# Optimization experiments

Measured on AMD Instinct MI355X. Metric: run time of the kernel, lower is better.

## Reference

```python
import jax, jax.numpy as jnp
import numpy as np

B, T, C = 4, 2048, 768   # batch, seq, n_embd
E, K = 8, 2              # n_routed_experts, moe_top_k (expert hidden dim == C per source)


def setup_inputs() -> dict:
    key = jax.random.key(0)
    ks = jax.random.split(key, 6)
    s = 0.02  # init scale to keep relu(x)^2 well-behaved
    return {
        "x": jax.random.normal(ks[0], (B, T, C), jnp.float32),
        "w_fc_sh": jax.random.normal(ks[1], (C, C), jnp.float32) * s,    # shared expert c_fc (stored [in,out])
        "w_proj_sh": jax.random.normal(ks[2], (C, C), jnp.float32) * s,  # shared expert c_proj
        "w1": jax.random.normal(ks[3], (E, C, C), jnp.float32) * s,      # routed experts c_fc, [E,in,out]
        "w2": jax.random.normal(ks[4], (E, C, C), jnp.float32) * s,      # routed experts c_proj
        "router_w": jax.random.normal(ks[5], (E, C), jnp.float32) * s,   # router weight [E, C]
        "balance_bias": jnp.zeros((E,), jnp.float32),                    # router balance_bias buffer
    }


def _mlp(x, wfc, wproj):
    # MLP: c_proj(relu(c_fc(x))**2)
    h = jnp.square(jax.nn.relu(x @ wfc))
    return h @ wproj


def reference(x, w_fc_sh, w_proj_sh, w1, w2, router_w, balance_bias):
    Bx, Tx, Cx = x.shape
    shared = _mlp(x, w_fc_sh, w_proj_sh)                    # [B,T,C]

    xf = x.reshape(-1, Cx)                                  # [N,C]
    # --- router ---
    logits = xf.astype(jnp.float32) @ router_w.T            # [N,E]
    scores = jax.nn.sigmoid(logits)
    _, idx = jax.lax.top_k(scores + balance_bias, K)        # selection uses biased scores
    tw = jnp.take_along_axis(scores, idx, axis=-1)          # gate weights from unbiased scores
    tw = tw / (tw.sum(-1, keepdims=True) + 1e-20)           # [N,K]

    # per-token per-expert combine weights (equivalent to gather/MLP/index_add loop)
    combine = (jax.nn.one_hot(idx, E, dtype=tw.dtype) * tw[..., None]).sum(1)  # [N,E]

    # dense all-expert compute, masked combine (same math as sparse dispatch)
    h = jnp.square(jax.nn.relu(jnp.einsum('nc,ech->neh', xf, w1)))  # [N,E,H]
    y = jnp.einsum('neh,ehc->nec', h, w2)                            # [N,E,C]
    routed = jnp.einsum('nec,ne->nc', y, combine)                    # [N,C]

    return shared + routed.reshape(Bx, Tx, Cx)
```

## Files before the change

kernel.cpp:

```cpp
#include <hip/hip_runtime.h>
#include <stdint.h>

#define N_TOK 8192
#define C_DIM 768
#define E_NUM 8
#define NT32 24
#define TOTX3 104
#define GRID3 312
#define XXP3 13

typedef short short8 __attribute__((ext_vector_type(8)));
typedef __bf16 bf16x8 __attribute__((ext_vector_type(8)));
typedef float f32x4 __attribute__((ext_vector_type(4)));

static __device__ __forceinline__ unsigned short f2bf(float f) {
    unsigned u = __float_as_uint(f);
    unsigned r = u + 0x7FFFu + ((u >> 16) & 1u);
    return (unsigned short)(r >> 16);
}
static __device__ __forceinline__ float bf2f(unsigned short h) {
    return __uint_as_float(((unsigned)h) << 16);
}

__global__ void wtrans_kernel(const float* __restrict__ wfc, const float* __restrict__ wpj,
                              const float* __restrict__ w1, const float* __restrict__ w2,
                              unsigned short* __restrict__ Wt) {
    __shared__ float tile[32][33];
    const int m = blockIdx.z;
    const float* src = (m == 0) ? wfc : (m == 1) ? wpj
                     : (m < 10) ? (w1 + (size_t)(m - 2) * C_DIM * C_DIM)
                                : (w2 + (size_t)(m - 10) * C_DIM * C_DIM);
    const int i0 = blockIdx.y * 32;
    const int o0 = blockIdx.x * 32;
    #pragma unroll
    for (int rr = 0; rr < 32; rr += 8)
        tile[threadIdx.y + rr][threadIdx.x] = src[(size_t)(i0 + threadIdx.y + rr) * C_DIM + o0 + threadIdx.x];
    __syncthreads();
    unsigned short* dst = Wt + (size_t)m * C_DIM * C_DIM;
    #pragma unroll
    for (int rr = 0; rr < 32; rr += 8) {
        int o = o0 + threadIdx.y + rr;
        dst[(size_t)o * C_DIM + i0 + threadIdx.x] = f2bf(tile[threadIdx.x][threadIdx.y + rr]);
    }
}

__global__ void router_kernel(const float* __restrict__ x, const float* __restrict__ rw,
                              const float* __restrict__ bias,
                              float* __restrict__ topk_w, int* __restrict__ eids,
                              unsigned short* __restrict__ xb) {
    const int wave = threadIdx.x >> 6;
    const int lane = threadIdx.x & 63;
    const int n = blockIdx.x * 4 + wave;
    const float* xp = x + (size_t)n * C_DIM + lane * 12;
    float xv[12];
    #pragma unroll
    for (int j = 0; j < 12; j++) xv[j] = xp[j];
    unsigned short* xbp = xb + (size_t)n * C_DIM + lane * 12;
    #pragma unroll
    for (int j = 0; j < 12; j++) xbp[j] = f2bf(xv[j]);
    float acc[E_NUM];
    #pragma unroll
    for (int e = 0; e < E_NUM; e++) acc[e] = 0.f;
    #pragma unroll
    for (int e = 0; e < E_NUM; e++) {
        const float* wp = rw + (size_t)e * C_DIM + lane * 12;
        #pragma unroll
        for (int j = 0; j < 12; j++) acc[e] += xv[j] * wp[j];
    }
    #pragma unroll
    for (int e = 0; e < E_NUM; e++) {
        #pragma unroll
        for (int off = 32; off > 0; off >>= 1) acc[e] += __shfl_xor(acc[e], off, 64);
    }
    if (lane == 0) {
        float sc[E_NUM];
        #pragma unroll
        for (int e = 0; e < E_NUM; e++) sc[e] = 1.f / (1.f + expf(-acc[e]));
        int e0 = 0; float best = -1e30f;
        #pragma unroll
        for (int e = 0; e < E_NUM; e++) { float v = sc[e] + bias[e]; if (v > best) { best = v; e0 = e; } }
        int e1 = -1; float best1 = -1e30f;
        #pragma unroll
        for (int e = 0; e < E_NUM; e++) { if (e == e0) continue; float v = sc[e] + bias[e]; if (v > best1) { best1 = v; e1 = e; } }
        float w0 = sc[e0], w1 = sc[e1];
        float s = w0 + w1 + 1e-20f;
        w0 /= s; w1 /= s;
        topk_w[n * 2] = w0; topk_w[n * 2 + 1] = w1;
        eids[n * 2] = e0; eids[n * 2 + 1] = e1;
    }
}

__global__ __launch_bounds__(1024) void bucketize_kernel(const int* __restrict__ eids,
                                                         int* __restrict__ counts,
                                                         int* __restrict__ buckets) {
    const int e = blockIdx.x;
    const int t = threadIdx.x;
    const int wv = t >> 6, lane = t & 63;
    __shared__ int wave_tot[16];
    int running = 0;
    for (int start = 0; start < 2 * N_TOK; start += 1024) {
        const int i = start + t;
        const int f = (eids[i] == e) ? 1 : 0;
        unsigned long long mask = __ballot(f);
        int pre = __popcll(mask & ((1ull << lane) - 1ull));
        if (lane == 0) wave_tot[wv] = __popcll(mask);
        __syncthreads();
        int wbase = 0, tot = 0;
        #pragma unroll
        for (int j = 0; j < 16; j++) { int c = wave_tot[j]; tot += c; if (j < wv) wbase += c; }
        if (f) buckets[e * N_TOK + running + wbase + pre] = i;
        running += tot;
        __syncthreads();
    }
    if (t == 0) counts[e] = running;
}

__global__ void prefix_kernel(const int* __restrict__ counts, int* __restrict__ xoffs) {
    if (threadIdx.x == 0 && blockIdx.x == 0) {
        int a = 0;
        for (int z = 0; z < E_NUM; z++) { xoffs[z] = a; a += (counts[z] + 255) >> 8; }
        xoffs[E_NUM] = a;
        xoffs[E_NUM + 1] = a + 32;
    }
}

#define GLOAD_LDS(g, l) __builtin_amdgcn_global_load_lds((const __attribute__((address_space(1))) void*)(g), (__attribute__((address_space(3))) void*)(l), 16, 0, 0)
#define WAITVM(n) asm volatile("s_waitcnt vmcnt(" #n ")" ::: "memory")
#define SCHEDB() __builtin_amdgcn_sched_barrier(0)
#define BAR() __builtin_amdgcn_s_barrier()

template <int PHASE>
__global__ __launch_bounds__(512, 2) void gemm_all_kernel(const unsigned short* __restrict__ Adir,
                                                          const unsigned short* __restrict__ Agat,
                                                          const unsigned short* __restrict__ WtAll,
                                                          void* __restrict__ dstDir,
                                                          unsigned short* __restrict__ dstGat,
                                                          const int* __restrict__ counts,
                                                          const int* __restrict__ buckets,
                                                          const int* __restrict__ xoffs) {
    const int fid = blockIdx.x;
    const int xcd = fid & 7;
    const int i3 = fid >> 3;
    const int xx = xcd * XXP3 + i3 / 3;
    const int y = i3 % 3;
    int xo[10];
    #pragma unroll
    for (int i = 0; i < 10; i++) xo[i] = xoffs[i];
    if (xx >= xo[9]) return;
    int z = E_NUM, xl = xx - xo[8];
    #pragma unroll
    for (int zz = 0; zz < E_NUM; zz++)
        if (xx >= xo[zz] && xx < xo[zz + 1]) { z = zz; xl = xx - xo[zz]; }
    const bool sh = (z == E_NUM);
    const int rows = sh ? N_TOK : counts[z];
    const int r0 = xl * 256;
    const int c0 = y * 256;

    __shared__ __align__(16) unsigned short lds[4 * 16384];

    const int t = threadIdx.x;
    const int lane = t & 63;
    const int wv = t >> 6;
    const int wm = wv >> 2;
    const int wn = wv & 3;

    const int widx = sh ? (PHASE == 0 ? 0 : 1) : (PHASE == 0 ? 2 + z : 10 + z);
    const unsigned short* Bmat = WtAll + (size_t)widx * C_DIM * C_DIM;
    const int* bk = buckets + z * N_TOK;

    const int srow = t >> 2;
    const int scol = (((t & 3) ^ ((t >> 3) & 3)) * 8);
    int grow0, grow1;
    const unsigned short* Asrc;
    if (sh) {
        Asrc = Adir;
        grow0 = r0 + srow; grow1 = r0 + 128 + srow;
    } else {
        Asrc = Agat;
        int p0 = r0 + srow, p1 = r0 + 128 + srow;
        int e0v = bk[p0 < rows ? p0 : 0];
        int e1v = bk[p1 < rows ? p1 : 0];
        grow0 = (PHASE == 0) ? (e0v >> 1) : e0v;
        grow1 = (PHASE == 0) ? (e1v >> 1) : e1v;
    }
    const unsigned short* ap0 = Asrc + (size_t)grow0 * C_DIM + scol;
    const unsigned short* ap1 = Asrc + (size_t)grow1 * C_DIM + scol;
    const unsigned short* bp0 = Bmat + (size_t)(c0 + srow) * C_DIM + scol;
    const unsigned short* bp1 = Bmat + (size_t)(c0 + 128 + srow) * C_DIM + scol;

    f32x4 acc[8][4];
    #pragma unroll
    for (int i = 0; i < 8; i++)
        #pragma unroll
        for (int j = 0; j < 4; j++) acc[i][j] = (f32x4){0.f, 0.f, 0.f, 0.f};

    const int fr = lane & 15;
    const int fq = lane >> 4;
    const int ks = ((fq ^ ((fr >> 1) & 3)) * 8);

    #pragma unroll
    for (int p = 0; p < 3; ++p) {
        unsigned short* d = lds + p * 16384 + t * 8;
        const int ko = p * 32;
        GLOAD_LDS(ap0 + ko, d);
        GLOAD_LDS(ap1 + ko, d + 4096);
        GLOAD_LDS(bp0 + ko, d + 8192);
        GLOAD_LDS(bp1 + ko, d + 12288);
    }

    #pragma unroll
    for (int kt = 0; kt < NT32; ++kt) {
        if (kt + 2 < NT32)      { WAITVM(8); }
        else if (kt + 1 < NT32) { WAITVM(4); }
        else                    { WAITVM(0); }
        BAR();
        SCHEDB();
        if (kt + 3 < NT32) {
            unsigned short* d = lds + ((kt + 3) & 3) * 16384 + t * 8;
            const int ko = (kt + 3) * 32;
            GLOAD_LDS(ap0 + ko, d);
            GLOAD_LDS(ap1 + ko, d + 4096);
            GLOAD_LDS(bp0 + ko, d + 8192);
            GLOAD_LDS(bp1 + ko, d + 12288);
        }
        SCHEDB();
        const unsigned short* buf = lds + (kt & 3) * 16384;
        short8 bfr[4];
        #pragma unroll
        for (int j = 0; j < 4; j++)
            bfr[j] = *reinterpret_cast<const short8*>(buf + 8192 + (size_t)(wn * 64 + j * 16 + fr) * 32 + ks);
        __builtin_amdgcn_s_setprio(1);
        #pragma unroll
        for (int i = 0; i < 8; i++) {
            short8 a = *reinterpret_cast<const short8*>(buf + (size_t)(wm * 128 + i * 16 + fr) * 32 + ks);
            #pragma unroll
            for (int j = 0; j < 4; j++)
                acc[i][j] = __builtin_amdgcn_mfma_f32_16x16x32_bf16(
                    __builtin_bit_cast(bf16x8, a), __builtin_bit_cast(bf16x8, bfr[j]), acc[i][j], 0, 0, 0);
        }
        __builtin_amdgcn_s_setprio(0);
    }

    const int orow = r0 + wm * 128;
    const int ocol = c0 + wn * 64;
    if (sh) {
        if constexpr (PHASE == 0) {
            unsigned short* Hd = (unsigned short*)dstDir;
            #pragma unroll
            for (int i = 0; i < 8; i++)
                #pragma unroll
                for (int rr = 0; rr < 4; rr++) {
                    size_t base = (size_t)(orow + i * 16 + fq * 4 + rr) * C_DIM;
                    #pragma unroll
                    for (int j = 0; j < 4; j++) {
                        float v = acc[i][j][rr];
                        float rl = v > 0.f ? v : 0.f;
                        Hd[base + ocol + j * 16 + fr] = f2bf(rl * rl);
                    }
                }
        } else {
            float* od = (float*)dstDir;
            #pragma unroll
            for (int i = 0; i < 8; i++)
                #pragma unroll
                for (int rr = 0; rr < 4; rr++) {
                    size_t base = (size_t)(orow + i * 16 + fq * 4 + rr) * C_DIM;
                    #pragma unroll
                    for (int j = 0; j < 4; j++)
                        od[base + ocol + j * 16 + fr] = acc[i][j][rr];
                }
        }
    } else {
        #pragma unroll
        for (int i = 0; i < 8; i++)
            #pragma unroll
            for (int rr = 0; rr < 4; rr++) {
                int pos = orow + i * 16 + fq * 4 + rr;
                if (pos < rows) {
                    int ent = bk[pos];
                    size_t base = (size_t)ent * C_DIM;
                    #pragma unroll
                    for (int j = 0; j < 4; j++) {
                        float v = acc[i][j][rr];
                        if (PHASE == 0) {
                            float rl = v > 0.f ? v : 0.f;
                            dstGat[base + ocol + j * 16 + fr] = f2bf(rl * rl);
                        } else {
                            dstGat[base + ocol + j * 16 + fr] = f2bf(v);
                        }
                    }
                }
            }
    }
}

__global__ void combine_kernel(float* __restrict__ out, const unsigned short* __restrict__ Y,
                               const float* __restrict__ tw) {
    int idx = blockIdx.x * blockDim.x + threadIdx.x;
    const int per_row = C_DIM / 4;
    if (idx >= N_TOK * per_row) return;
    int n = idx / per_row;
    int c = (idx % per_row) * 4;
    float w0 = tw[n * 2], w1 = tw[n * 2 + 1];
    const ushort4 a = *reinterpret_cast<const ushort4*>(Y + (size_t)(n * 2) * C_DIM + c);
    const ushort4 b = *reinterpret_cast<const ushort4*>(Y + (size_t)(n * 2 + 1) * C_DIM + c);
    float4* op = reinterpret_cast<float4*>(out + (size_t)n * C_DIM + c);
    float4 o = *op;
    o.x += w0 * bf2f(a.x) + w1 * bf2f(b.x);
    o.y += w0 * bf2f(a.y) + w1 * bf2f(b.y);
    o.z += w0 * bf2f(a.z) + w1 * bf2f(b.z);
    o.w += w0 * bf2f(a.w) + w1 * bf2f(b.w);
    *op = o;
}

extern "C" void kernel_launch(void* const* d_in, const int* in_sizes, int n_in,
                              void* d_out, int out_size, void* d_ws, size_t ws_size,
                              hipStream_t stream) {
    const float* x   = (const float*)d_in[0];
    const float* wfc = (const float*)d_in[1];
    const float* wpj = (const float*)d_in[2];
    const float* w1  = (const float*)d_in[3];
    const float* w2  = (const float*)d_in[4];
    const float* rw  = (const float*)d_in[5];
    const float* bias= (const float*)d_in[6];
    float* out = (float*)d_out;

    char* ws = (char*)d_ws;
    size_t off = 0;
    auto alloc = [&](size_t bytes) { void* p = ws + off; off += (bytes + 255) & ~(size_t)255; return p; };
    unsigned short* xb   = (unsigned short*)alloc((size_t)N_TOK * C_DIM * 2);
    unsigned short* Wt   = (unsigned short*)alloc((size_t)18 * C_DIM * C_DIM * 2);
    unsigned short* H    = (unsigned short*)alloc((size_t)N_TOK * 2 * C_DIM * 2);
    unsigned short* Hsh  = (unsigned short*)alloc((size_t)N_TOK * C_DIM * 2);
    unsigned short* Y    = (unsigned short*)alloc((size_t)N_TOK * 2 * C_DIM * 2);
    float* topk_w        = (float*)alloc((size_t)N_TOK * 2 * 4);
    int* counts          = (int*)alloc(256);
    int* buckets         = (int*)alloc((size_t)E_NUM * N_TOK * 4);
    int* eids            = (int*)alloc((size_t)2 * N_TOK * 4);
    int* xoffs           = (int*)alloc(64);

    wtrans_kernel<<<dim3(24, 24, 18), dim3(32, 8), 0, stream>>>(wfc, wpj, w1, w2, Wt);
    router_kernel<<<N_TOK / 4, 256, 0, stream>>>(x, rw, bias, topk_w, eids, xb);
    bucketize_kernel<<<E_NUM, 1024, 0, stream>>>(eids, counts, buckets);
    prefix_kernel<<<1, 64, 0, stream>>>(counts, xoffs);

    gemm_all_kernel<0><<<GRID3, 512, 0, stream>>>(xb, xb, Wt, Hsh, H, counts, buckets, xoffs);
    gemm_all_kernel<1><<<GRID3, 512, 0, stream>>>(Hsh, H, Wt, out, Y, counts, buckets, xoffs);

    combine_kernel<<<(N_TOK * (C_DIM / 4) + 255) / 256, 256, 0, stream>>>(out, Y, topk_w);
}
```

Baseline: 158.5 us.

## Shrink GEMM tiles to 256x128 with double buffering; fuse prep and prefix kernels

The GEMM kernel now uses 256x128 output tiles with a two-stage LDS double buffer instead of 256x256 tiles with a four-deep pipeline. The grid doubles to 624 blocks and launch bounds allow four blocks per CU, trading less operand reuse and a wait-for-all vmcnt each k-step for more occupancy and better load balance. The weight transpose and router kernels are merged into one launch, and the expert-offset prefix is computed inside each GEMM block, which removes two kernel launches. Out-of-range gather rows now clamp to the last valid row instead of row 0.

```diff
diff --git a/kernel.cpp b/kernel.cpp
--- a/kernel.cpp
+++ b/kernel.cpp
@@ -4,10 +4,10 @@
 #define N_TOK 8192
 #define C_DIM 768
 #define E_NUM 8
-#define NT32 24
-#define TOTX3 104
-#define GRID3 312
-#define XXP3 13
+#define NTK 24
+#define GRIDG 624
+#define PREP_WT 10368
+#define PREP_TOT (PREP_WT + N_TOK / 4)
 
 typedef short short8 __attribute__((ext_vector_type(8)));
 typedef __bf16 bf16x8 __attribute__((ext_vector_type(8)));
@@ -22,71 +22,81 @@
     return __uint_as_float(((unsigned)h) << 16);
 }
 
-__global__ void wtrans_kernel(const float* __restrict__ wfc, const float* __restrict__ wpj,
-                              const float* __restrict__ w1, const float* __restrict__ w2,
-                              unsigned short* __restrict__ Wt) {
+__global__ __launch_bounds__(256) void prep_kernel(const float* __restrict__ wfc,
+                                                   const float* __restrict__ wpj,
+                                                   const float* __restrict__ w1,
+                                                   const float* __restrict__ w2,
+                                                   unsigned short* __restrict__ Wt,
+                                                   const float* __restrict__ x,
+                                                   const float* __restrict__ rw,
+                                                   const float* __restrict__ bias,
+                                                   float* __restrict__ topk_w,
+                                                   int* __restrict__ eids,
+                                                   unsigned short* __restrict__ xb) {
     __shared__ float tile[32][33];
-    const int m = blockIdx.z;
-    const float* src = (m == 0) ? wfc : (m == 1) ? wpj
-                     : (m < 10) ? (w1 + (size_t)(m - 2) * C_DIM * C_DIM)
-                                : (w2 + (size_t)(m - 10) * C_DIM * C_DIM);
-    const int i0 = blockIdx.y * 32;
-    const int o0 = blockIdx.x * 32;
-    #pragma unroll
-    for (int rr = 0; rr < 32; rr += 8)
-        tile[threadIdx.y + rr][threadIdx.x] = src[(size_t)(i0 + threadIdx.y + rr) * C_DIM + o0 + threadIdx.x];
-    __syncthreads();
-    unsigned short* dst = Wt + (size_t)m * C_DIM * C_DIM;
-    #pragma unroll
-    for (int rr = 0; rr < 32; rr += 8) {
-        int o = o0 + threadIdx.y + rr;
-        dst[(size_t)o * C_DIM + i0 + threadIdx.x] = f2bf(tile[threadIdx.x][threadIdx.y + rr]);
-    }
-}
-
-__global__ void router_kernel(const float* __restrict__ x, const float* __restrict__ rw,
-                              const float* __restrict__ bias,
-                              float* __restrict__ topk_w, int* __restrict__ eids,
-                              unsigned short* __restrict__ xb) {
-    const int wave = threadIdx.x >> 6;
-    const int lane = threadIdx.x & 63;
-    const int n = blockIdx.x * 4 + wave;
-    const float* xp = x + (size_t)n * C_DIM + lane * 12;
-    float xv[12];
-    #pragma unroll
-    for (int j = 0; j < 12; j++) xv[j] = xp[j];
-    unsigned short* xbp = xb + (size_t)n * C_DIM + lane * 12;
-    #pragma unroll
-    for (int j = 0; j < 12; j++) xbp[j] = f2bf(xv[j]);
-    float acc[E_NUM];
-    #pragma unroll
-    for (int e = 0; e < E_NUM; e++) acc[e] = 0.f;
-    #pragma unroll
-    for (int e = 0; e < E_NUM; e++) {
-        const float* wp = rw + (size_t)e * C_DIM + lane * 12;
-        #pragma unroll
-        for (int j = 0; j < 12; j++) acc[e] += xv[j] * wp[j];
-    }
-    #pragma unroll
-    for (int e = 0; e < E_NUM; e++) {
-        #pragma unroll
-        for (int off = 32; off > 0; off >>= 1) acc[e] += __shfl_xor(acc[e], off, 64);
-    }
-    if (lane == 0) {
-        float sc[E_NUM];
-        #pragma unroll
-        for (int e = 0; e < E_NUM; e++) sc[e] = 1.f / (1.f + expf(-acc[e]));
-        int e0 = 0; float best = -1e30f;
-        #pragma unroll
-        for (int e = 0; e < E_NUM; e++) { float v = sc[e] + bias[e]; if (v > best) { best = v; e0 = e; } }
-        int e1 = -1; float best1 = -1e30f;
-        #pragma unroll
-        for (int e = 0; e < E_NUM; e++) { if (e == e0) continue; float v = sc[e] + bias[e]; if (v > best1) { best1 = v; e1 = e; } }
-        float w0 = sc[e0], w1 = sc[e1];
-        float s = w0 + w1 + 1e-20f;
-        w0 /= s; w1 /= s;
-        topk_w[n * 2] = w0; topk_w[n * 2 + 1] = w1;
-        eids[n * 2] = e0; eids[n * 2 + 1] = e1;
+    const int bx = blockIdx.x;
+    const int t = threadIdx.x;
+    if (bx < PREP_WT) {
+        const int m = bx / 576;
+        const int rem = bx - m * 576;
+        const int i0 = (rem / 24) * 32;
+        const int o0 = (rem % 24) * 32;
+        const int tx = t & 31, ty = t >> 5;
+        const float* src = (m == 0) ? wfc : (m == 1) ? wpj
+                         : (m < 10) ? (w1 + (size_t)(m - 2) * C_DIM * C_DIM)
+                                    : (w2 + (size_t)(m - 10) * C_DIM * C_DIM);
+        #pragma unroll
+        for (int rr = 0; rr < 32; rr += 8)
+            tile[ty + rr][tx] = src[(size_t)(i0 + ty + rr) * C_DIM + o0 + tx];
+        __syncthreads();
+        unsigned short* dst = Wt + (size_t)m * C_DIM * C_DIM;
+        #pragma unroll
+        for (int rr = 0; rr < 32; rr += 8) {
+            int o = o0 + ty + rr;
+            dst[(size_t)o * C_DIM + i0 + tx] = f2bf(tile[tx][ty + rr]);
+        }
+    } else {
+        const int rb = bx - PREP_WT;
+        const int wave = t >> 6;
+        const int lane = t & 63;
+        const int n = rb * 4 + wave;
+        const float* xp = x + (size_t)n * C_DIM + lane * 12;
+        float xv[12];
+        #pragma unroll
+        for (int j = 0; j < 12; j++) xv[j] = xp[j];
+        unsigned short* xbp = xb + (size_t)n * C_DIM + lane * 12;
+        #pragma unroll
+        for (int j = 0; j < 12; j++) xbp[j] = f2bf(xv[j]);
+        float acc[E_NUM];
+        #pragma unroll
+        for (int e = 0; e < E_NUM; e++) acc[e] = 0.f;
+        #pragma unroll
+        for (int e = 0; e < E_NUM; e++) {
+            const float* wp = rw + (size_t)e * C_DIM + lane * 12;
+            #pragma unroll
+            for (int j = 0; j < 12; j++) acc[e] += xv[j] * wp[j];
+        }
+        #pragma unroll
+        for (int e = 0; e < E_NUM; e++) {
+            #pragma unroll
+            for (int off = 32; off > 0; off >>= 1) acc[e] += __shfl_xor(acc[e], off, 64);
+        }
+        if (lane == 0) {
+            float sc[E_NUM];
+            #pragma unroll
+            for (int e = 0; e < E_NUM; e++) sc[e] = 1.f / (1.f + expf(-acc[e]));
+            int e0 = 0; float best = -1e30f;
+            #pragma unroll
+            for (int e = 0; e < E_NUM; e++) { float v = sc[e] + bias[e]; if (v > best) { best = v; e0 = e; } }
+            int e1 = -1; float best1 = -1e30f;
+            #pragma unroll
+            for (int e = 0; e < E_NUM; e++) { if (e == e0) continue; float v = sc[e] + bias[e]; if (v > best1) { best1 = v; e1 = e; } }
+            float w0 = sc[e0], w1 = sc[e1];
+            float s = w0 + w1 + 1e-20f;
+            w0 /= s; w1 /= s;
+            topk_w[n * 2] = w0; topk_w[n * 2 + 1] = w1;
+            eids[n * 2] = e0; eids[n * 2 + 1] = e1;
+        }
     }
 }
 
@@ -115,82 +125,78 @@
     if (t == 0) counts[e] = running;
 }
 
-__global__ void prefix_kernel(const int* __restrict__ counts, int* __restrict__ xoffs) {
-    if (threadIdx.x == 0 && blockIdx.x == 0) {
-        int a = 0;
-        for (int z = 0; z < E_NUM; z++) { xoffs[z] = a; a += (counts[z] + 255) >> 8; }
-        xoffs[E_NUM] = a;
-        xoffs[E_NUM + 1] = a + 32;
-    }
-}
-
 #define GLOAD_LDS(g, l) __builtin_amdgcn_global_load_lds((const __attribute__((address_space(1))) void*)(g), (__attribute__((address_space(3))) void*)(l), 16, 0, 0)
-#define WAITVM(n) asm volatile("s_waitcnt vmcnt(" #n ")" ::: "memory")
+#define WAITVM0() asm volatile("s_waitcnt vmcnt(0)" ::: "memory")
 #define SCHEDB() __builtin_amdgcn_sched_barrier(0)
 #define BAR() __builtin_amdgcn_s_barrier()
 
 template <int PHASE>
-__global__ __launch_bounds__(512, 2) void gemm_all_kernel(const unsigned short* __restrict__ Adir,
+__global__ __launch_bounds__(512, 4) void gemm_all_kernel(const unsigned short* __restrict__ Adir,
                                                           const unsigned short* __restrict__ Agat,
                                                           const unsigned short* __restrict__ WtAll,
                                                           void* __restrict__ dstDir,
                                                           unsigned short* __restrict__ dstGat,
                                                           const int* __restrict__ counts,
-                                                          const int* __restrict__ buckets,
-                                                          const int* __restrict__ xoffs) {
+                                                          const int* __restrict__ buckets) {
     const int fid = blockIdx.x;
     const int xcd = fid & 7;
-    const int i3 = fid >> 3;
-    const int xx = xcd * XXP3 + i3 / 3;
-    const int y = i3 % 3;
-    int xo[10];
+    const int i6 = fid >> 3;
+    const int xx = xcd + 8 * (i6 / 6);
+    const int y = i6 % 6;
+    int cz[E_NUM];
     #pragma unroll
-    for (int i = 0; i < 10; i++) xo[i] = xoffs[i];
-    if (xx >= xo[9]) return;
-    int z = E_NUM, xl = xx - xo[8];
+    for (int zz = 0; zz < E_NUM; zz++) cz[zz] = counts[zz];
+    int xo[E_NUM + 1]; int a = 0;
     #pragma unroll
-    for (int zz = 0; zz < E_NUM; zz++)
-        if (xx >= xo[zz] && xx < xo[zz + 1]) { z = zz; xl = xx - xo[zz]; }
-    const bool sh = (z == E_NUM);
-    const int rows = sh ? N_TOK : counts[z];
+    for (int zz = 0; zz < E_NUM; zz++) { xo[zz] = a; a += (cz[zz] + 255) >> 8; }
+    xo[E_NUM] = a;
+    if (xx >= a + 32) return;
+    const bool sh = (xx >= a);
+    int z = 0, xl = xx - a;
+    if (!sh) {
+        #pragma unroll
+        for (int zz = 0; zz < E_NUM; zz++)
+            if (xx >= xo[zz] && xx < xo[zz + 1]) { z = zz; xl = xx - xo[zz]; }
+    }
+    const int rows = sh ? N_TOK : cz[z];
     const int r0 = xl * 256;
-    const int c0 = y * 256;
-
-    __shared__ __align__(16) unsigned short lds[4 * 16384];
+    const int c0 = y * 128;
+
+    __shared__ __align__(16) unsigned short lds[2 * 12288];
 
     const int t = threadIdx.x;
     const int lane = t & 63;
     const int wv = t >> 6;
-    const int wm = wv >> 2;
-    const int wn = wv & 3;
+    const int wm = wv >> 1;
+    const int wn = wv & 1;
 
     const int widx = sh ? (PHASE == 0 ? 0 : 1) : (PHASE == 0 ? 2 + z : 10 + z);
     const unsigned short* Bmat = WtAll + (size_t)widx * C_DIM * C_DIM;
     const int* bk = buckets + z * N_TOK;
 
-    const int srow = t >> 2;
-    const int scol = (((t & 3) ^ ((t >> 3) & 3)) * 8);
-    int grow0, grow1;
+    const int scol = (((lane & 3) ^ ((lane >> 3) & 3)) * 8);
+    const int rA0 = wv * 16 + (lane >> 2);
+    const int rA1 = 128 + rA0;
+    int g0, g1;
     const unsigned short* Asrc;
     if (sh) {
         Asrc = Adir;
-        grow0 = r0 + srow; grow1 = r0 + 128 + srow;
+        g0 = r0 + rA0; g1 = r0 + rA1;
     } else {
         Asrc = Agat;
-        int p0 = r0 + srow, p1 = r0 + 128 + srow;
-        int e0v = bk[p0 < rows ? p0 : 0];
-        int e1v = bk[p1 < rows ? p1 : 0];
-        grow0 = (PHASE == 0) ? (e0v >> 1) : e0v;
-        grow1 = (PHASE == 0) ? (e1v >> 1) : e1v;
-    }
-    const unsigned short* ap0 = Asrc + (size_t)grow0 * C_DIM + scol;
-    const unsigned short* ap1 = Asrc + (size_t)grow1 * C_DIM + scol;
-    const unsigned short* bp0 = Bmat + (size_t)(c0 + srow) * C_DIM + scol;
-    const unsigned short* bp1 = Bmat + (size_t)(c0 + 128 + srow) * C_DIM + scol;
-
-    f32x4 acc[8][4];
+        int p0 = r0 + rA0, p1 = r0 + rA1;
+        int e0v = bk[p0 < rows ? p0 : rows - 1];
+        int e1v = bk[p1 < rows ? p1 : rows - 1];
+        g0 = (PHASE == 0) ? (e0v >> 1) : e0v;
+        g1 = (PHASE == 0) ? (e1v >> 1) : e1v;
+    }
+    const unsigned short* ap0 = Asrc + (size_t)g0 * C_DIM + scol;
+    const unsigned short* ap1 = Asrc + (size_t)g1 * C_DIM + scol;
+    const unsigned short* bp  = Bmat + (size_t)(c0 + rA0) * C_DIM + scol;
+
+    f32x4 acc[4][4];
     #pragma unroll
-    for (int i = 0; i < 8; i++)
+    for (int i = 0; i < 4; i++)
         #pragma unroll
         for (int j = 0; j < 4; j++) acc[i][j] = (f32x4){0.f, 0.f, 0.f, 0.f};
 
@@ -198,56 +204,48 @@
     const int fq = lane >> 4;
     const int ks = ((fq ^ ((fr >> 1) & 3)) * 8);
 
+    GLOAD_LDS(ap0, lds + wv * 512 + lane * 8);
+    GLOAD_LDS(ap1, lds + 4096 + wv * 512 + lane * 8);
+    GLOAD_LDS(bp,  lds + 8192 + wv * 512 + lane * 8);
+
     #pragma unroll
-    for (int p = 0; p < 3; ++p) {
-        unsigned short* d = lds + p * 16384 + t * 8;
-        const int ko = p * 32;
-        GLOAD_LDS(ap0 + ko, d);
-        GLOAD_LDS(ap1 + ko, d + 4096);
-        GLOAD_LDS(bp0 + ko, d + 8192);
-        GLOAD_LDS(bp1 + ko, d + 12288);
-    }
-
-    #pragma unroll
-    for (int kt = 0; kt < NT32; ++kt) {
-        if (kt + 2 < NT32)      { WAITVM(8); }
-        else if (kt + 1 < NT32) { WAITVM(4); }
-        else                    { WAITVM(0); }
+    for (int kt = 0; kt < NTK; ++kt) {
+        WAITVM0();
         BAR();
         SCHEDB();
-        if (kt + 3 < NT32) {
-            unsigned short* d = lds + ((kt + 3) & 3) * 16384 + t * 8;
-            const int ko = (kt + 3) * 32;
-            GLOAD_LDS(ap0 + ko, d);
-            GLOAD_LDS(ap1 + ko, d + 4096);
-            GLOAD_LDS(bp0 + ko, d + 8192);
-            GLOAD_LDS(bp1 + ko, d + 12288);
+        if (kt + 1 < NTK) {
+            unsigned short* d = lds + ((kt + 1) & 1) * 12288;
+            const int ko = (kt + 1) * 32;
+            GLOAD_LDS(ap0 + ko, d + wv * 512 + lane * 8);
+            GLOAD_LDS(ap1 + ko, d + 4096 + wv * 512 + lane * 8);
+            GLOAD_LDS(bp + ko,  d + 8192 + wv * 512 + lane * 8);
         }
         SCHEDB();
-        const unsigned short* buf = lds + (kt & 3) * 16384;
-        short8 bfr[4];
+        const unsigned short* buf = lds + (kt & 1) * 12288;
+        short8 afr[4], bfr[4];
+        #pragma unroll
+        for (int i = 0; i < 4; i++)
+            afr[i] = *reinterpret_cast<const short8*>(buf + (size_t)(wm * 64 + i * 16 + fr) * 32 + ks);
         #pragma unroll
         for (int j = 0; j < 4; j++)
             bfr[j] = *reinterpret_cast<const short8*>(buf + 8192 + (size_t)(wn * 64 + j * 16 + fr) * 32 + ks);
         __builtin_amdgcn_s_setprio(1);
         #pragma unroll
-        for (int i = 0; i < 8; i++) {
-            short8 a = *reinterpret_cast<const short8*>(buf + (size_t)(wm * 128 + i * 16 + fr) * 32 + ks);
+        for (int i = 0; i < 4; i++)
             #pragma unroll
             for (int j = 0; j < 4; j++)
                 acc[i][j] = __builtin_amdgcn_mfma_f32_16x16x32_bf16(
-                    __builtin_bit_cast(bf16x8, a), __builtin_bit_cast(bf16x8, bfr[j]), acc[i][j], 0, 0, 0);
-        }
+                    __builtin_bit_cast(bf16x8, afr[i]), __builtin_bit_cast(bf16x8, bfr[j]), acc[i][j], 0, 0, 0);
         __builtin_amdgcn_s_setprio(0);
     }
 
-    const int orow = r0 + wm * 128;
+    const int orow = r0 + wm * 64;
     const int ocol = c0 + wn * 64;
     if (sh) {
         if constexpr (PHASE == 0) {
             unsigned short* Hd = (unsigned short*)dstDir;
             #pragma unroll
-            for (int i = 0; i < 8; i++)
+            for (int i = 0; i < 4; i++)
                 #pragma unroll
                 for (int rr = 0; rr < 4; rr++) {
                     size_t base = (size_t)(orow + i * 16 + fq * 4 + rr) * C_DIM;
@@ -261,7 +259,7 @@
         } else {
             float* od = (float*)dstDir;
             #pragma unroll
-            for (int i = 0; i < 8; i++)
+            for (int i = 0; i < 4; i++)
                 #pragma unroll
                 for (int rr = 0; rr < 4; rr++) {
                     size_t base = (size_t)(orow + i * 16 + fq * 4 + rr) * C_DIM;
@@ -272,7 +270,7 @@
         }
     } else {
         #pragma unroll
-        for (int i = 0; i < 8; i++)
+        for (int i = 0; i < 4; i++)
             #pragma unroll
             for (int rr = 0; rr < 4; rr++) {
                 int pos = orow + i * 16 + fq * 4 + rr;
@@ -337,15 +335,12 @@
     int* counts          = (int*)alloc(256);
     int* buckets         = (int*)alloc((size_t)E_NUM * N_TOK * 4);
     int* eids            = (int*)alloc((size_t)2 * N_TOK * 4);
-    int* xoffs           = (int*)alloc(64);
-
-    wtrans_kernel<<<dim3(24, 24, 18), dim3(32, 8), 0, stream>>>(wfc, wpj, w1, w2, Wt);
-    router_kernel<<<N_TOK / 4, 256, 0, stream>>>(x, rw, bias, topk_w, eids, xb);
+
+    prep_kernel<<<PREP_TOT, 256, 0, stream>>>(wfc, wpj, w1, w2, Wt, x, rw, bias, topk_w, eids, xb);
     bucketize_kernel<<<E_NUM, 1024, 0, stream>>>(eids, counts, buckets);
-    prefix_kernel<<<1, 64, 0, stream>>>(counts, xoffs);
-
-    gemm_all_kernel<0><<<GRID3, 512, 0, stream>>>(xb, xb, Wt, Hsh, H, counts, buckets, xoffs);
-    gemm_all_kernel<1><<<GRID3, 512, 0, stream>>>(Hsh, H, Wt, out, Y, counts, buckets, xoffs);
+
+    gemm_all_kernel<0><<<GRIDG, 512, 0, stream>>>(xb, xb, Wt, Hsh, H, counts, buckets);
+    gemm_all_kernel<1><<<GRIDG, 512, 0, stream>>>(Hsh, H, Wt, out, Y, counts, buckets);
 
     combine_kernel<<<(N_TOK * (C_DIM / 4) + 255) / 256, 256, 0, stream>>>(out, Y, topk_w);
 }
```

After: 145.2 us. 8.4% less time.
